# Kernel tuning notes

Hardware: AMD Instinct MI355X
Metric: run time of the kernel (lower is better)

The kernel has to match this reference:

```python
import jax, jax.numpy as jnp
import numpy as np

S = 3        # message passing steps
L = 128      # latent size
N = 10000    # nodes
E = 160000   # edges
DN, DE, DG = 64, 16, 8
OUT = 8
EPS = 1e-5


def _ln(x, scale, offset):
    m = jnp.mean(x, axis=-1, keepdims=True)
    v = jnp.var(x, axis=-1, keepdims=True)
    return (x - m) * jax.lax.rsqrt(v + EPS) * scale + offset


def _mlp(x, W0, b0, W1, b1):
    h = jax.nn.relu(x @ W0 + b0)
    return jax.nn.relu(h @ W1 + b1)


def setup_inputs() -> dict:
    key = jax.random.key(0)
    ks = iter(jax.random.split(key, 64))

    def w(shape, fan_in):
        return jax.random.normal(next(ks), shape, jnp.float32) / np.sqrt(fan_in).astype(np.float32)

    inp = {
        "nodes": jax.random.normal(next(ks), (N, DN), jnp.float32),
        "edges": jax.random.normal(next(ks), (E, DE), jnp.float32),
        "globals_": jax.random.normal(next(ks), (1, DG), jnp.float32),
        "senders": jax.random.randint(next(ks), (E,), 0, N),
        "receivers": jax.random.randint(next(ks), (E,), 0, N),
        # embedder
        "emb_node_W": w((DN, L), DN), "emb_node_b": jnp.zeros((L,), jnp.float32),
        "emb_edge_W": w((DE, L), DE), "emb_edge_b": jnp.zeros((L,), jnp.float32),
        "emb_glob_W": w((DG, L), DG), "emb_glob_b": jnp.zeros((L,), jnp.float32),
        # per-step MLPs (2 layers each)
        "edge_W0": w((S, 4 * L, L), 4 * L), "edge_b0": jnp.zeros((S, L), jnp.float32),
        "edge_W1": w((S, L, L), L),         "edge_b1": jnp.zeros((S, L), jnp.float32),
        "node_W0": w((S, 4 * L, L), 4 * L), "node_b0": jnp.zeros((S, L), jnp.float32),
        "node_W1": w((S, L, L), L),         "node_b1": jnp.zeros((S, L), jnp.float32),
        "glob_W0": w((S, 3 * L, L), 3 * L), "glob_b0": jnp.zeros((S, L), jnp.float32),
        "glob_W1": w((S, L, L), L),         "glob_b1": jnp.zeros((S, L), jnp.float32),
        # per-step layernorm (0: nodes, 1: edges, 2: globals)
        "ln_scale": jnp.ones((S, 3, L), jnp.float32),
        "ln_offset": jnp.zeros((S, 3, L), jnp.float32),
        # decoder (globals only)
        "dec_W": w((L, OUT), L), "dec_b": jnp.zeros((OUT,), jnp.float32),
    }
    return inp


def reference(nodes, edges, globals_, senders, receivers,
              emb_node_W, emb_node_b, emb_edge_W, emb_edge_b, emb_glob_W, emb_glob_b,
              edge_W0, edge_b0, edge_W1, edge_b1,
              node_W0, node_b0, node_W1, node_b1,
              glob_W0, glob_b0, glob_W1, glob_b1,
              ln_scale, ln_offset, dec_W, dec_b):
    # embed to latent
    n = nodes @ emb_node_W + emb_node_b      # [N, L]
    e = edges @ emb_edge_W + emb_edge_b      # [E, L]
    g = globals_ @ emb_glob_W + emb_glob_b   # [1, L]

    for s in range(S):
        # edge update: concat(edges, nodes[senders], nodes[receivers], globals)
        g_e = jnp.broadcast_to(g, (e.shape[0], L))
        e_in = jnp.concatenate([e, n[senders], n[receivers], g_e], axis=-1)  # [E, 4L]
        e_new = _mlp(e_in, edge_W0[s], edge_b0[s], edge_W1[s], edge_b1[s])
        # node update: concat(nodes, segsum(e,senders), segsum(e,receivers), globals)
        sent_agg = jax.ops.segment_sum(e_new, senders, num_segments=N)
        recv_agg = jax.ops.segment_sum(e_new, receivers, num_segments=N)
        g_n = jnp.broadcast_to(g, (N, L))
        n_in = jnp.concatenate([n, sent_agg, recv_agg, g_n], axis=-1)  # [N, 4L]
        n_new = _mlp(n_in, node_W0[s], node_b0[s], node_W1[s], node_b1[s])
        # global update: concat(node_agg, edge_agg, globals) (single graph)
        node_agg = jnp.sum(n_new, axis=0, keepdims=True)
        edge_agg = jnp.sum(e_new, axis=0, keepdims=True)
        g_in = jnp.concatenate([node_agg, edge_agg, g], axis=-1)  # [1, 3L]
        g_new = _mlp(g_in, glob_W0[s], glob_b0[s], glob_W1[s], glob_b1[s])
        # residual + layernorm
        n = _ln(n_new + n, ln_scale[s, 0], ln_offset[s, 0])
        e = _ln(e_new + e, ln_scale[s, 1], ln_offset[s, 1])
        g = _ln(g_new + g, ln_scale[s, 2], ln_offset[s, 2])

    # decoder maps globals only
    return g @ dec_W + dec_b  # [1, OUT]
```

## Files before the change

### kernel.cpp

```cpp
#include <hip/hip_runtime.h>
#include <hip/hip_bf16.h>

typedef __bf16 bf16;
typedef __bf16 bf16x8 __attribute__((ext_vector_type(8)));
typedef __bf16 bf16x4 __attribute__((ext_vector_type(4)));
typedef float  f32x4  __attribute__((ext_vector_type(4)));

#define NL 128
#define NN 10000
#define NE 160000
#define LN_EPS 1e-5f

__device__ __forceinline__ f32x4 f4zero() {
    f32x4 v; v[0] = 0.f; v[1] = 0.f; v[2] = 0.f; v[3] = 0.f; return v;
}

__device__ __forceinline__ int swz_off(int row, int b) {
    return row * 256 + (b ^ ((row & 7) << 4));
}

__device__ __forceinline__ bf16x8 frag_ld(const bf16* base, int row, int kbyte) {
    return *reinterpret_cast<const bf16x8*>(
        reinterpret_cast<const char*>(base) + swz_off(row, kbyte));
}

template <int NT>
__device__ __forceinline__ void stage_img(const bf16* __restrict__ img, bf16* dst, int tid) {
    #pragma unroll
    for (int i = 0; i < 2048 / NT; ++i) {
        int byte = (i * NT + tid) * 16;
        *reinterpret_cast<bf16x8*>(reinterpret_cast<char*>(dst) + byte) =
            *reinterpret_cast<const bf16x8*>(reinterpret_cast<const char*>(img) + byte);
    }
}

template <int NT>
__device__ __forceinline__ void stage_img_ld(const bf16* __restrict__ img, bf16x8* r, int tid) {
    #pragma unroll
    for (int i = 0; i < 2048 / NT; ++i)
        r[i] = *reinterpret_cast<const bf16x8*>(reinterpret_cast<const char*>(img) +
                                                (i * NT + tid) * 16);
}
template <int NT>
__device__ __forceinline__ void stage_img_st(bf16* dst, const bf16x8* r, int tid) {
    #pragma unroll
    for (int i = 0; i < 2048 / NT; ++i)
        *reinterpret_cast<bf16x8*>(reinterpret_cast<char*>(dst) + (i * NT + tid) * 16) = r[i];
}

__device__ __forceinline__ void stage_rows16(const float* __restrict__ src0, bf16* sX,
                                             int wrow0, int lane) {
    int c8 = (lane & 15) * 8;
    #pragma unroll
    for (int i = 0; i < 4; ++i) {
        int sub = i * 4 + (lane >> 4);
        const float* src = src0 + (size_t)sub * 128 + c8;
        f32x4 a = *reinterpret_cast<const f32x4*>(src);
        f32x4 b = *reinterpret_cast<const f32x4*>(src + 4);
        bf16x8 v;
        v[0] = (bf16)a[0]; v[1] = (bf16)a[1]; v[2] = (bf16)a[2]; v[3] = (bf16)a[3];
        v[4] = (bf16)b[0]; v[5] = (bf16)b[1]; v[6] = (bf16)b[2]; v[7] = (bf16)b[3];
        *reinterpret_cast<bf16x8*>(reinterpret_cast<char*>(sX) + swz_off(wrow0 + sub, c8 * 2)) = v;
    }
}

__device__ __forceinline__ void mfma_16x128(const bf16* sA, const bf16* sB, int arow, int kq,
                                            f32x4 acc[8]) {
    #pragma unroll
    for (int kk = 0; kk < 4; ++kk) {
        bf16x8 af = frag_ld(sA, arow, kk * 64 + kq);
        #pragma unroll
        for (int t = 0; t < 8; ++t) {
            bf16x8 bfr = frag_ld(sB, t * 16 + (arow & 15), kk * 64 + kq);
            acc[t] = __builtin_amdgcn_mfma_f32_16x16x32_bf16(af, bfr, acc[t], 0, 0, 0);
        }
    }
}

__device__ __forceinline__ void acc_to_lds_bf16(bf16* sX, const f32x4 acc[8], int w, int lane) {
    int c0 = lane & 15;
    #pragma unroll
    for (int r = 0; r < 4; ++r) {
        int rl = w * 16 + (lane >> 4) * 4 + r;
        #pragma unroll
        for (int t = 0; t < 8; ++t) {
            int col = t * 16 + c0;
            *reinterpret_cast<bf16*>(reinterpret_cast<char*>(sX) + swz_off(rl, col * 2)) =
                (bf16)acc[t][r];
        }
    }
}

__device__ __forceinline__ void lds_rows_to_global_bf16(const bf16* sX, bf16* __restrict__ dst0,
                                                        int w, int lane) {
    int c8 = (lane & 15) * 8;
    #pragma unroll
    for (int i = 0; i < 4; ++i) {
        int sub = i * 4 + (lane >> 4);
        bf16x8 v = *reinterpret_cast<const bf16x8*>(
            reinterpret_cast<const char*>(sX) + swz_off(w * 16 + sub, c8 * 2));
        *reinterpret_cast<bf16x8*>(dst0 + (size_t)sub * 128 + c8) = v;
    }
}

__global__ void k_prep(const float* __restrict__ eW0, const float* __restrict__ eW1,
                       const float* __restrict__ nW0, const float* __restrict__ nW1,
                       bf16* __restrict__ imgs, const float* __restrict__ globals_,
                       const float* __restrict__ embW, const float* __restrict__ embB,
                       float* __restrict__ g, const float* __restrict__ eb0,
                       const float* __restrict__ nb0, float* __restrict__ gve,
                       float* __restrict__ gvn, int* __restrict__ deg,
                       float* __restrict__ eagg, float* __restrict__ nagg,
                       int* __restrict__ done) {
    const int b = blockIdx.x;
    const int tid = threadIdx.x;
    if (b < 24) {
        const int s = b >> 3, kind = b & 7;
        const float* src;
        if (kind < 3)       src = eW0 + (size_t)s * 512 * 128 + (size_t)kind * 128 * 128;
        else if (kind == 3) src = eW1 + (size_t)s * 128 * 128;
        else if (kind < 7)  src = nW0 + (size_t)s * 512 * 128 + (size_t)(kind - 4) * 128 * 128;
        else                src = nW1 + (size_t)s * 128 * 128;
        bf16* img = imgs + (size_t)b * 16384;
        for (int i = 0; i < 16; ++i) {
            int q = tid + i * 256;
            int col = q & 127;
            int k0 = (q >> 7) << 2;
            bf16x4 v;
            v[0] = (bf16)src[(k0 + 0) * 128 + col];
            v[1] = (bf16)src[(k0 + 1) * 128 + col];
            v[2] = (bf16)src[(k0 + 2) * 128 + col];
            v[3] = (bf16)src[(k0 + 3) * 128 + col];
            *reinterpret_cast<bf16x4*>(reinterpret_cast<char*>(img) + swz_off(col, k0 * 2)) = v;
        }
    } else if (b == 24) {
        __shared__ float sG[128];
        if (tid < 3) done[tid] = 0;
        if (tid < 128) {
            float a = embB[tid];
            #pragma unroll
            for (int k = 0; k < 8; ++k) a += globals_[k] * embW[k * 128 + tid];
            g[tid] = a;
            sG[tid] = a;
        }
        __syncthreads();
        if (tid < 128) {
            const float* eW0g = eW0 + 384 * 128;
            const float* nW0g = nW0 + 384 * 128;
            float ae = eb0[tid], an = nb0[tid];
            for (int k = 0; k < 128; ++k) {
                float gv = sG[k];
                ae += gv * eW0g[k * 128 + tid];
                an += gv * nW0g[k * 128 + tid];
            }
            gve[tid] = ae;
            gvn[tid] = an;
        }
    } else {
        for (int i = tid; i < 2 * NN; i += 256) deg[i] = 0;
        for (int i = tid; i < 8 * 128; i += 256) eagg[i] = 0.f;
        for (int i = tid; i < 4 * 128; i += 256) nagg[i] = 0.f;
    }
}


__global__ void k_hist(const int* __restrict__ senders, const int* __restrict__ receivers,
                       int* __restrict__ deg_s, int* __restrict__ deg_r) {
    int i = blockIdx.x * 256 + threadIdx.x;
    if (i < NE) {
        atomicAdd(&deg_s[senders[i]], 1);
        atomicAdd(&deg_r[receivers[i]], 1);
    }
}

__device__ void scan_arr(const int* __restrict__ deg, int* __restrict__ rs, int* __restrict__ cur,
                         int* sW, int* sRun) {
    const int tid = threadIdx.x, lane = tid & 63, wid = tid >> 6;
    if (tid == 0) *sRun = 0;
    __syncthreads();
    for (int base = 0; base < NN; base += 1024) {
        int i = base + tid;
        int orig = (i < NN) ? deg[i] : 0;
        int v = orig;
        #pragma unroll
        for (int off = 1; off < 64; off <<= 1) {
            int u = __shfl_up(v, off, 64);
            if (lane >= off) v += u;
        }
        if (lane == 63) sW[wid] = v;
        __syncthreads();
        if (wid == 0 && lane < 16) {
            int u = sW[lane];
            #pragma unroll
            for (int off = 1; off < 16; off <<= 1) {
                int t = __shfl_up(u, off, 16);
                if (lane >= off) u += t;
            }
            sW[lane] = u;
        }
        __syncthreads();
        int waveoff = (wid == 0) ? 0 : sW[wid - 1];
        int incl = v + waveoff + *sRun;
        if (i < NN) {
            rs[i + 1] = incl;
            cur[i] = incl - orig;
        }
        __syncthreads();
        if (tid == 1023) *sRun = incl;
        __syncthreads();
    }
    if (tid == 0) rs[0] = 0;
}

__global__ void k_scan(const int* __restrict__ deg_s, int* __restrict__ rs_s,
                       int* __restrict__ cur_s, const int* __restrict__ deg_r,
                       int* __restrict__ rs_r, int* __restrict__ cur_r) {
    __shared__ int sW[16];
    __shared__ int sRun;
    scan_arr(deg_s, rs_s, cur_s, sW, &sRun);
    __syncthreads();
    scan_arr(deg_r, rs_r, cur_r, sW, &sRun);
}

__global__ void k_scatter_s(const int* __restrict__ senders, const int* __restrict__ receivers,
                            int* __restrict__ cur_s, int* __restrict__ perm,
                            int* __restrict__ snd_s, int* __restrict__ rcv_s) {
    int i = blockIdx.x * 256 + threadIdx.x;
    if (i < NE) {
        int s = senders[i];
        int p = atomicAdd(&cur_s[s], 1);
        perm[p] = i;
        snd_s[p] = s;
        rcv_s[p] = receivers[i];
    }
}

__global__ void k_scatter_r(const int* __restrict__ rcv_s, int* __restrict__ cur_r,
                            int* __restrict__ csr_r) {
    int j = blockIdx.x * 256 + threadIdx.x;
    if (j < NE) {
        int r = rcv_s[j];
        int p = atomicAdd(&cur_r[r], 1);
        csr_r[p] = j;
    }
}


__global__ __launch_bounds__(256, 2) void k_embed_nodes(
    const float* __restrict__ nodes, const float* __restrict__ W, const float* __restrict__ b,
    float* __restrict__ n_out, const bf16* __restrict__ imgPs, const bf16* __restrict__ imgPr,
    bf16* __restrict__ nsW, bf16* __restrict__ nrW) {
    __shared__ __align__(16) char smem[81920];
    float* sWemb = (float*)smem;
    float* sB = (float*)(smem + 32768);
    bf16* sWa = (bf16*)smem;
    bf16* sWb = (bf16*)(smem + 32768);
    bf16* sX = (bf16*)(smem + 65536);
    const int tid = threadIdx.x;
    const int lane = tid & 63;
    const int w = tid >> 6;
    const int rowbase = blockIdx.x * 64;
    const bool wvalid = (rowbase + w * 16) < NN;

    for (int i = tid; i < 64 * 128; i += 256) sWemb[i] = W[i];
    if (tid < 128) sB[tid] = b[tid];
    __syncthreads();
    const int col = tid & 127;
    const int rh = tid >> 7;
    for (int i = 0; i < 32; ++i) {
        int row = rowbase + i * 2 + rh;
        if (row < NN) {
            const f32x4* x4 = reinterpret_cast<const f32x4*>(nodes + (size_t)row * 64);
            float a = sB[col];
            #pragma unroll
            for (int k4 = 0; k4 < 16; ++k4) {
                f32x4 xv = x4[k4];
                a += xv[0] * sWemb[(k4 * 4 + 0) * 128 + col];
                a += xv[1] * sWemb[(k4 * 4 + 1) * 128 + col];
                a += xv[2] * sWemb[(k4 * 4 + 2) * 128 + col];
                a += xv[3] * sWemb[(k4 * 4 + 3) * 128 + col];
            }
            n_out[(size_t)row * 128 + col] = a;
            *reinterpret_cast<bf16*>(reinterpret_cast<char*>(sX) +
                                     swz_off(i * 2 + rh, col * 2)) = (bf16)a;
        }
    }
    __syncthreads();
    stage_img<256>(imgPs, sWa, tid);
    stage_img<256>(imgPr, sWb, tid);
    __syncthreads();
    if (!wvalid) return;

    const int arow = w * 16 + (lane & 15);
    const int kq = (lane >> 4) * 16;
    f32x4 acc[8], acc2[8];
    #pragma unroll
    for (int t = 0; t < 8; ++t) { acc[t] = f4zero(); acc2[t] = f4zero(); }
    mfma_16x128(sX, sWa, arow, kq, acc);
    mfma_16x128(sX, sWb, arow, kq, acc2);

    acc_to_lds_bf16(sX, acc, w, lane);
    lds_rows_to_global_bf16(sX, nsW + (size_t)(rowbase + w * 16) * 128, w, lane);
    acc_to_lds_bf16(sX, acc2, w, lane);
    lds_rows_to_global_bf16(sX, nrW + (size_t)(rowbase + w * 16) * 128, w, lane);
}

__global__ void k_embed_edges(const float* __restrict__ edges, const int* __restrict__ perm,
                              const float* __restrict__ W, const float* __restrict__ b,
                              bf16* __restrict__ e_out) {
    __shared__ float sW[16 * 128];
    __shared__ float sB[128];
    const int tid = threadIdx.x;
    for (int i = tid; i < 16 * 128; i += 256) sW[i] = W[i];
    if (tid < 128) sB[tid] = b[tid];
    __syncthreads();
    const int col = tid & 127;
    const int rh = tid >> 7;
    const int rowbase = blockIdx.x * 128;
    for (int i = 0; i < 64; ++i) {
        int row = rowbase + i * 2 + rh;
        int src = perm[row];
        const float* x = edges + (size_t)src * 16;
        float a = sB[col];
        #pragma unroll
        for (int k = 0; k < 16; ++k) a += x[k] * sW[k * 128 + col];
        e_out[(size_t)row * 128 + col] = (bf16)a;
    }
}


__global__ __launch_bounds__(512, 2) void k_edge(
    bf16* e_rw, bf16* __restrict__ e_new_out, const bf16* __restrict__ nsW,
    const bf16* __restrict__ nrW, float* __restrict__ edge_agg,
    const int* __restrict__ snd_s, const int* __restrict__ rcv_s,
    const bf16* __restrict__ imgW0, const bf16* __restrict__ imgW1,
    const float* __restrict__ gvec, const float* __restrict__ b1,
    const float* __restrict__ lnS, const float* __restrict__ lnO) {
    __shared__ __align__(16) char smem[65536];
    bf16* sW = (bf16*)smem;
    bf16* sX = (bf16*)(smem + 32768);
    float* sEagg = (float*)smem;

    const int tid = threadIdx.x;
    const int lane = tid & 63;
    const int w = tid >> 6;
    const int rowbase = blockIdx.x * 128;
    const int arow = w * 16 + (lane & 15);
    const int kq = (lane >> 4) * 16;
    const int c0 = lane & 15;
    const int qrt = lane >> 4;
    const int c8 = c0 * 8;

    stage_img<512>(imgW0, sW, tid);

    int snd_i[4], rcv_i[4];
    bf16x8 eold8[4];
    #pragma unroll
    for (int i = 0; i < 4; ++i) {
        int gr = rowbase + w * 16 + i * 4 + qrt;
        snd_i[i] = snd_s[gr];
        rcv_i[i] = rcv_s[gr];
        eold8[i] = *reinterpret_cast<const bf16x8*>(e_rw + (size_t)gr * 128 + c8);
    }

    f32x4 gvA = *reinterpret_cast<const f32x4*>(gvec + c8);
    f32x4 gvB = *reinterpret_cast<const f32x4*>(gvec + c8 + 4);
    f32x4 lsA = *reinterpret_cast<const f32x4*>(lnS + c8);
    f32x4 lsB = *reinterpret_cast<const f32x4*>(lnS + c8 + 4);
    f32x4 loA = *reinterpret_cast<const f32x4*>(lnO + c8);
    f32x4 loB = *reinterpret_cast<const f32x4*>(lnO + c8 + 4);
    float bb[8];
    #pragma unroll
    for (int t = 0; t < 8; ++t) bb[t] = b1[t * 16 + c0];

    bf16x8 ns8[4], nr8[4];
    #pragma unroll
    for (int i = 0; i < 4; ++i) {
        ns8[i] = *reinterpret_cast<const bf16x8*>(nsW + (size_t)snd_i[i] * 128 + c8);
        nr8[i] = *reinterpret_cast<const bf16x8*>(nrW + (size_t)rcv_i[i] * 128 + c8);
    }

    #pragma unroll
    for (int i = 0; i < 4; ++i)
        *reinterpret_cast<bf16x8*>(reinterpret_cast<char*>(sX) +
                                   swz_off(w * 16 + i * 4 + qrt, c8 * 2)) = eold8[i];

    __syncthreads();

    f32x4 acc[8];
    #pragma unroll
    for (int t = 0; t < 8; ++t) acc[t] = f4zero();
    __builtin_amdgcn_s_setprio(1);
    mfma_16x128(sX, sW, arow, kq, acc);
    __builtin_amdgcn_s_setprio(0);

    __syncthreads();

    bf16x8 w1r[4];
    stage_img_ld<512>(imgW1, w1r, tid);

    #pragma unroll
    for (int r = 0; r < 4; ++r) {
        int rl = w * 16 + (lane >> 4) * 4 + r;
        #pragma unroll
        for (int t = 0; t < 8; ++t)
            *reinterpret_cast<bf16*>(reinterpret_cast<char*>(sX) +
                                     swz_off(rl, (t * 16 + c0) * 2)) = (bf16)acc[t][r];
    }
    #pragma unroll
    for (int i = 0; i < 4; ++i) {
        int rl = w * 16 + i * 4 + qrt;
        bf16x8 a8 = *reinterpret_cast<const bf16x8*>(
            reinterpret_cast<const char*>(sX) + swz_off(rl, c8 * 2));
        bf16x8 h8;
        #pragma unroll
        for (int j = 0; j < 8; ++j) {
            float gvj = (j < 4) ? gvA[j] : gvB[j - 4];
            float v = (float)a8[j] + (float)ns8[i][j] + (float)nr8[i][j] + gvj;
            h8[j] = (bf16)fmaxf(v, 0.f);
        }
        *reinterpret_cast<bf16x8*>(reinterpret_cast<char*>(sX) + swz_off(rl, c8 * 2)) = h8;
    }

    stage_img_st<512>(sW, w1r, tid);
    __syncthreads();

    f32x4 acc2[8];
    #pragma unroll
    for (int t = 0; t < 8; ++t) acc2[t] = f4zero();
    __builtin_amdgcn_s_setprio(1);
    mfma_16x128(sX, sW, arow, kq, acc2);
    __builtin_amdgcn_s_setprio(0);

    #pragma unroll
    for (int r = 0; r < 4; ++r) {
        int rl = w * 16 + (lane >> 4) * 4 + r;
        #pragma unroll
        for (int t = 0; t < 8; ++t)
            *reinterpret_cast<bf16*>(reinterpret_cast<char*>(sX) +
                                     swz_off(rl, (t * 16 + c0) * 2)) =
                (bf16)fmaxf(acc2[t][r] + bb[t], 0.f);
    }

    float cs[8];
    #pragma unroll
    for (int j = 0; j < 8; ++j) cs[j] = 0.f;
    bf16* enew0 = e_new_out + (size_t)rowbase * 128;
    bf16* e0 = e_rw + (size_t)rowbase * 128;
    #pragma unroll
    for (int i = 0; i < 4; ++i) {
        int sub = w * 16 + i * 4 + qrt;
        bf16x8 en8 = *reinterpret_cast<const bf16x8*>(
            reinterpret_cast<const char*>(sX) + swz_off(sub, c8 * 2));
        *reinterpret_cast<bf16x8*>(enew0 + (size_t)sub * 128 + c8) = en8;
        float rv[8], s1 = 0.f, s2 = 0.f;
        #pragma unroll
        for (int j = 0; j < 8; ++j) {
            float en = (float)en8[j];
            cs[j] += en;
            float v = en + (float)eold8[i][j];
            rv[j] = v;
            s1 += v;
            s2 += v * v;
        }
        #pragma unroll
        for (int off = 1; off < 16; off <<= 1) {
            s1 += __shfl_xor(s1, off, 16);
            s2 += __shfl_xor(s2, off, 16);
        }
        float mean = s1 * (1.f / 128.f);
        float rstd = rsqrtf(s2 * (1.f / 128.f) - mean * mean + LN_EPS);
        bf16x8 o8;
        #pragma unroll
        for (int j = 0; j < 8; ++j) {
            float ls = (j < 4) ? lsA[j] : lsB[j - 4];
            float lo = (j < 4) ? loA[j] : loB[j - 4];
            o8[j] = (bf16)((rv[j] - mean) * rstd * ls + lo);
        }
        *reinterpret_cast<bf16x8*>(e0 + (size_t)sub * 128 + c8) = o8;
    }

    #pragma unroll
    for (int j = 0; j < 8; ++j) {
        cs[j] += __shfl_xor(cs[j], 16, 64);
        cs[j] += __shfl_xor(cs[j], 32, 64);
    }
    __syncthreads();
    if (qrt == 0) {
        float* dst = sEagg + w * 128 + c8;
        #pragma unroll
        for (int j = 0; j < 8; ++j) dst[j] = cs[j];
    }
    __syncthreads();
    if (tid < 128) {
        float v = 0.f;
        #pragma unroll
        for (int ww = 0; ww < 8; ++ww) v += sEagg[ww * 128 + tid];
        atomicAdd(&edge_agg[(blockIdx.x & 7) * 128 + tid], v);
    }
}

__global__ __launch_bounds__(256, 2) void k_node(
    float* n_rw, const bf16* __restrict__ e_new, const int* __restrict__ rs_s,
    const int* __restrict__ rs_r, const int* __restrict__ csr_r,
    float* __restrict__ node_agg , const bf16* __restrict__ imgW0,
    const bf16* __restrict__ imgW1, const float* __restrict__ gvec,
    const float* __restrict__ b1, const float* __restrict__ lnS,
    const float* __restrict__ lnO, const bf16* __restrict__ imgPs,
    const bf16* __restrict__ imgPr, bf16* __restrict__ nsW, bf16* __restrict__ nrW,
    int do_proj,
    int* __restrict__ done_ctr, float* __restrict__ edge_agg , float* __restrict__ g,
    const float* __restrict__ gW0, const float* __restrict__ gb0,
    const float* __restrict__ gW1, const float* __restrict__ gb1,
    const float* __restrict__ glnS, const float* __restrict__ glnO,
    const float* __restrict__ eW0g, const float* __restrict__ eb0n,
    const float* __restrict__ nW0g, const float* __restrict__ nb0n,
    float* __restrict__ gve, float* __restrict__ gvn, const float* __restrict__ decW,
    const float* __restrict__ decb, float* __restrict__ out, int do_next, int do_dec) {
    __shared__ __align__(16) char smem[81920];
    __shared__ int sLast;
    bf16* sA = (bf16*)smem;
    bf16* sB = (bf16*)(smem + 32768);
    bf16* sX = (bf16*)(smem + 65536);
    float* sNagg = (float*)smem;

    const int tid = threadIdx.x;
    const int lane = tid & 63;
    const int w = tid >> 6;
    const int rowbase = blockIdx.x * 64;
    const bool wvalid = (rowbase + w * 16) < NN;
    const int arow = w * 16 + (lane & 15);
    const int kq = (lane >> 4) * 16;
    const int c0 = lane & 15;
    const int qrt = lane >> 4;
    const int c8 = c0 * 8;

    stage_img<256>(imgW0, sA, tid);
    stage_img<256>(imgW0 + 16384, sB, tid);
    if (wvalid) stage_rows16(n_rw + (size_t)(rowbase + w * 16) * 128, sX, w * 16, lane);
    __syncthreads();

    float gvf[8], bbf[8];
    #pragma unroll
    for (int t = 0; t < 8; ++t) {
        gvf[t] = gvec[t * 16 + c0];
        bbf[t] = b1[t * 16 + c0];
    }
    f32x4 lsA4 = *reinterpret_cast<const f32x4*>(lnS + c8);
    f32x4 lsB4 = *reinterpret_cast<const f32x4*>(lnS + c8 + 4);
    f32x4 loA4 = *reinterpret_cast<const f32x4*>(lnO + c8);
    f32x4 loB4 = *reinterpret_cast<const f32x4*>(lnO + c8 + 4);

    f32x4 acc[8];
    #pragma unroll
    for (int t = 0; t < 8; ++t) acc[t] = f4zero();
    float cs[8];
    #pragma unroll
    for (int j = 0; j < 8; ++j) cs[j] = 0.f;

    if (wvalid) mfma_16x128(sX, sA, arow, kq, acc);
    __syncthreads();

    stage_img<256>(imgW0 + 32768, sA, tid);
    if (wvalid) {
        #pragma unroll
        for (int i = 0; i < 4; ++i) {
            int node = rowbase + w * 16 + i * 4 + qrt;
            float a[8];
            #pragma unroll
            for (int j = 0; j < 8; ++j) a[j] = 0.f;
            int jb = rs_s[node], je = rs_s[node + 1];
            int jj = jb;
            for (; jj + 3 < je; jj += 4) {
                bf16x8 v0 = *reinterpret_cast<const bf16x8*>(e_new + (size_t)(jj + 0) * 128 + c8);
                bf16x8 v1 = *reinterpret_cast<const bf16x8*>(e_new + (size_t)(jj + 1) * 128 + c8);
                bf16x8 v2 = *reinterpret_cast<const bf16x8*>(e_new + (size_t)(jj + 2) * 128 + c8);
                bf16x8 v3 = *reinterpret_cast<const bf16x8*>(e_new + (size_t)(jj + 3) * 128 + c8);
                #pragma unroll
                for (int j = 0; j < 8; ++j)
                    a[j] += (float)v0[j] + (float)v1[j] + (float)v2[j] + (float)v3[j];
            }
            for (; jj < je; ++jj) {
                bf16x8 v = *reinterpret_cast<const bf16x8*>(e_new + (size_t)jj * 128 + c8);
                #pragma unroll
                for (int j = 0; j < 8; ++j) a[j] += (float)v[j];
            }
            bf16x8 o;
            #pragma unroll
            for (int j = 0; j < 8; ++j) o[j] = (bf16)a[j];
            *reinterpret_cast<bf16x8*>(reinterpret_cast<char*>(sX) +
                                       swz_off(w * 16 + i * 4 + qrt, c8 * 2)) = o;
        }
        mfma_16x128(sX, sB, arow, kq, acc);
    }
    __syncthreads();

    stage_img<256>(imgW1, sB, tid);
    if (wvalid) {
        #pragma unroll
        for (int i = 0; i < 4; ++i) {
            int node = rowbase + w * 16 + i * 4 + qrt;
            float a[8];
            #pragma unroll
            for (int j = 0; j < 8; ++j) a[j] = 0.f;
            int pb = rs_r[node], pe = rs_r[node + 1];
            int pp = pb;
            for (; pp + 3 < pe; pp += 4) {
                int j0 = csr_r[pp], j1 = csr_r[pp + 1], j2 = csr_r[pp + 2], j3 = csr_r[pp + 3];
                bf16x8 v0 = *reinterpret_cast<const bf16x8*>(e_new + (size_t)j0 * 128 + c8);
                bf16x8 v1 = *reinterpret_cast<const bf16x8*>(e_new + (size_t)j1 * 128 + c8);
                bf16x8 v2 = *reinterpret_cast<const bf16x8*>(e_new + (size_t)j2 * 128 + c8);
                bf16x8 v3 = *reinterpret_cast<const bf16x8*>(e_new + (size_t)j3 * 128 + c8);
                #pragma unroll
                for (int j = 0; j < 8; ++j)
                    a[j] += (float)v0[j] + (float)v1[j] + (float)v2[j] + (float)v3[j];
            }
            for (; pp < pe; ++pp) {
                int j0 = csr_r[pp];
                bf16x8 v = *reinterpret_cast<const bf16x8*>(e_new + (size_t)j0 * 128 + c8);
                #pragma unroll
                for (int j = 0; j < 8; ++j) a[j] += (float)v[j];
            }
            bf16x8 o;
            #pragma unroll
            for (int j = 0; j < 8; ++j) o[j] = (bf16)a[j];
            *reinterpret_cast<bf16x8*>(reinterpret_cast<char*>(sX) +
                                       swz_off(w * 16 + i * 4 + qrt, c8 * 2)) = o;
        }
        mfma_16x128(sX, sA, arow, kq, acc);

        #pragma unroll
        for (int r = 0; r < 4; ++r) {
            int rl = w * 16 + (lane >> 4) * 4 + r;
            #pragma unroll
            for (int t = 0; t < 8; ++t)
                *reinterpret_cast<bf16*>(reinterpret_cast<char*>(sX) +
                                         swz_off(rl, (t * 16 + c0) * 2)) =
                    (bf16)fmaxf(acc[t][r] + gvf[t], 0.f);
        }
    }
    __syncthreads();

    if (wvalid) {
        #pragma unroll
        for (int t = 0; t < 8; ++t) acc[t] = f4zero();
        mfma_16x128(sX, sB, arow, kq, acc);
        #pragma unroll
        for (int r = 0; r < 4; ++r) {
            int rl = w * 16 + (lane >> 4) * 4 + r;
            #pragma unroll
            for (int t = 0; t < 8; ++t)
                *reinterpret_cast<bf16*>(reinterpret_cast<char*>(sX) +
                                         swz_off(rl, (t * 16 + c0) * 2)) =
                    (bf16)fmaxf(acc[t][r] + bbf[t], 0.f);
        }

        const float* nbase = n_rw + (size_t)(rowbase + w * 16) * 128;
        #pragma unroll
        for (int i = 0; i < 4; ++i) {
            int sub = i * 4 + qrt;
            bf16x8 en8 = *reinterpret_cast<const bf16x8*>(
                reinterpret_cast<const char*>(sX) + swz_off(w * 16 + sub, c8 * 2));
            f32x4 noA = *reinterpret_cast<const f32x4*>(nbase + (size_t)sub * 128 + c8);
            f32x4 noB = *reinterpret_cast<const f32x4*>(nbase + (size_t)sub * 128 + c8 + 4);
            float rv[8], s1 = 0.f, s2 = 0.f;
            #pragma unroll
            for (int j = 0; j < 8; ++j) {
                float en = (float)en8[j];
                cs[j] += en;
                float v = en + ((j < 4) ? noA[j] : noB[j - 4]);
                rv[j] = v;
                s1 += v;
                s2 += v * v;
            }
            #pragma unroll
            for (int off = 1; off < 16; off <<= 1) {
                s1 += __shfl_xor(s1, off, 16);
                s2 += __shfl_xor(s2, off, 16);
            }
            float mean = s1 * (1.f / 128.f);
            float rstd = rsqrtf(s2 * (1.f / 128.f) - mean * mean + LN_EPS);
            f32x4 oA, oB;
            bf16x8 l8;
            #pragma unroll
            for (int j = 0; j < 8; ++j) {
                float ls = (j < 4) ? lsA4[j] : lsB4[j - 4];
                float lo = (j < 4) ? loA4[j] : loB4[j - 4];
                float o = (rv[j] - mean) * rstd * ls + lo;
                if (j < 4) oA[j] = o; else oB[j - 4] = o;
                l8[j] = (bf16)o;
            }
            float* orow = n_rw + (size_t)(rowbase + w * 16 + sub) * 128 + c8;
            *reinterpret_cast<f32x4*>(orow) = oA;
            *reinterpret_cast<f32x4*>(orow + 4) = oB;
            *reinterpret_cast<bf16x8*>(reinterpret_cast<char*>(sX) +
                                       swz_off(w * 16 + sub, c8 * 2)) = l8;
        }
    }

    if (do_proj) {
        __syncthreads();
        stage_img<256>(imgPs, sA, tid);
        stage_img<256>(imgPr, sB, tid);
        __syncthreads();
        if (wvalid) {
            f32x4 pa[8], pb[8];
            #pragma unroll
            for (int t = 0; t < 8; ++t) { pa[t] = f4zero(); pb[t] = f4zero(); }
            mfma_16x128(sX, sA, arow, kq, pa);
            mfma_16x128(sX, sB, arow, kq, pb);
            acc_to_lds_bf16(sX, pa, w, lane);
            lds_rows_to_global_bf16(sX, nsW + (size_t)(rowbase + w * 16) * 128, w, lane);
            acc_to_lds_bf16(sX, pb, w, lane);
            lds_rows_to_global_bf16(sX, nrW + (size_t)(rowbase + w * 16) * 128, w, lane);
        }
    }

    #pragma unroll
    for (int j = 0; j < 8; ++j) {
        cs[j] += __shfl_xor(cs[j], 16, 64);
        cs[j] += __shfl_xor(cs[j], 32, 64);
    }
    __syncthreads();
    if (qrt == 0) {
        float* dst = sNagg + w * 128 + c8;
        #pragma unroll
        for (int j = 0; j < 8; ++j) dst[j] = wvalid ? cs[j] : 0.f;
    }
    __syncthreads();
    if (tid < 128) {
        float v = sNagg[tid] + sNagg[128 + tid] + sNagg[256 + tid] + sNagg[384 + tid];
        atomicAdd(&node_agg[(blockIdx.x & 3) * 128 + tid], v);
    }

    __syncthreads();
    if (tid == 0) {
        __threadfence();
        int old = atomicAdd(done_ctr, 1);
        sLast = (old == (int)gridDim.x - 1);
    }
    __syncthreads();
    if (!sLast) return;

    float* sIn = (float*)smem;
    float* sP0 = sIn + 384;
    float* sP1 = sP0 + 128;
    float* sH = sP1 + 128;
    float* sG = sH + 128;
    float* sMR = sG + 128;
    const int j = tid & 127;
    const int part = tid >> 7;

    if (tid < 128) {
        float v = 0.f;
        #pragma unroll
        for (int c = 0; c < 4; ++c) v += atomicAdd(&node_agg[c * 128 + tid], 0.f);
        #pragma unroll
        for (int c = 0; c < 4; ++c) atomicExch(&node_agg[c * 128 + tid], 0.f);
        sIn[tid] = v;
        sIn[256 + tid] = g[tid];
    } else {
        float v = 0.f;
        #pragma unroll
        for (int c = 0; c < 8; ++c) v += edge_agg[c * 128 + j];
        #pragma unroll
        for (int c = 0; c < 8; ++c) edge_agg[c * 128 + j] = 0.f;
        sIn[128 + j] = v;
    }
    __syncthreads();
    {
        float p = 0.f;
        for (int k = 0; k < 192; ++k) {
            int kk = part * 192 + k;
            p += sIn[kk] * gW0[(size_t)kk * 128 + j];
        }
        (part ? sP1 : sP0)[j] = p;
    }
    __syncthreads();
    if (tid < 128) sH[tid] = fmaxf(gb0[tid] + sP0[tid] + sP1[tid], 0.f);
    __syncthreads();
    {
        float p = 0.f;
        for (int k = 0; k < 64; ++k) {
            int kk = part * 64 + k;
            p += sH[kk] * gW1[(size_t)kk * 128 + j];
        }
        (part ? sP1 : sP0)[j] = p;
    }
    __syncthreads();
    float res = 0.f;
    if (tid < 128) {
        res = fmaxf(gb1[tid] + sP0[tid] + sP1[tid], 0.f) + sIn[256 + tid];
        sP0[tid] = res;
        sP1[tid] = res * res;
    }
    __syncthreads();
    if (tid < 64) {
        float a = sP0[tid] + sP0[tid + 64];
        float q = sP1[tid] + sP1[tid + 64];
        #pragma unroll
        for (int off = 1; off < 64; off <<= 1) {
            a += __shfl_xor(a, off, 64);
            q += __shfl_xor(q, off, 64);
        }
        if (tid == 0) {
            float m = a * (1.f / 128.f);
            float v = q * (1.f / 128.f) - m * m;
            sMR[0] = m;
            sMR[1] = rsqrtf(v + LN_EPS);
        }
    }
    __syncthreads();
    if (tid < 128) {
        float go = (res - sMR[0]) * sMR[1] * glnS[tid] + glnO[tid];
        g[tid] = go;
        sG[tid] = go;
    }
    __syncthreads();
    if (do_next) {
        float pe = 0.f, pn = 0.f;
        for (int k = 0; k < 64; ++k) {
            int kk = part * 64 + k;
            float gv = sG[kk];
            pe += gv * eW0g[(size_t)kk * 128 + j];
            pn += gv * nW0g[(size_t)kk * 128 + j];
        }
        (part ? sP1 : sP0)[j] = pe;
        sIn[part * 128 + j] = pn;
        __syncthreads();
        if (tid < 128) {
            gve[tid] = eb0n[tid] + sP0[tid] + sP1[tid];
            gvn[tid] = nb0n[tid] + sIn[tid] + sIn[128 + tid];
        }
    }
    if (do_dec && tid < 8) {
        float a = decb[tid];
        for (int k = 0; k < 128; ++k) a += sG[k] * decW[k * 8 + tid];
        out[tid] = a;
    }
}

extern "C" void kernel_launch(void* const* d_in, const int* in_sizes, int n_in, void* d_out,
                              int out_size, void* d_ws, size_t ws_size, hipStream_t stream) {
    (void)in_sizes; (void)n_in; (void)out_size; (void)ws_size;
    const float* nodes = (const float*)d_in[0];
    const float* edges = (const float*)d_in[1];
    const float* globals_ = (const float*)d_in[2];
    const int* senders = (const int*)d_in[3];
    const int* receivers = (const int*)d_in[4];
    const float* emb_node_W = (const float*)d_in[5];
    const float* emb_node_b = (const float*)d_in[6];
    const float* emb_edge_W = (const float*)d_in[7];
    const float* emb_edge_b = (const float*)d_in[8];
    const float* emb_glob_W = (const float*)d_in[9];
    const float* emb_glob_b = (const float*)d_in[10];
    const float* edge_W0 = (const float*)d_in[11];
    const float* edge_b0 = (const float*)d_in[12];
    const float* edge_W1 = (const float*)d_in[13];
    const float* edge_b1 = (const float*)d_in[14];
    const float* node_W0 = (const float*)d_in[15];
    const float* node_b0 = (const float*)d_in[16];
    const float* node_W1 = (const float*)d_in[17];
    const float* node_b1 = (const float*)d_in[18];
    const float* glob_W0 = (const float*)d_in[19];
    const float* glob_b0 = (const float*)d_in[20];
    const float* glob_W1 = (const float*)d_in[21];
    const float* glob_b1 = (const float*)d_in[22];
    const float* ln_scale = (const float*)d_in[23];
    const float* ln_offset = (const float*)d_in[24];
    const float* dec_W = (const float*)d_in[25];
    const float* dec_b = (const float*)d_in[26];

    char* ws = (char*)d_ws;
    size_t off = 0;
    auto alloc = [&](size_t bytes) -> char* {
        char* p = ws + off;
        off += (bytes + 255) & ~(size_t)255;
        return p;
    };
    bf16* e = (bf16*)alloc((size_t)NE * NL * 2);
    bf16* e_new = (bf16*)alloc((size_t)NE * NL * 2);
    float* n = (float*)alloc((size_t)NN * NL * 4);
    bf16* nsW = (bf16*)alloc((size_t)NN * NL * 2);
    bf16* nrW = (bf16*)alloc((size_t)NN * NL * 2);
    bf16* imgs = (bf16*)alloc((size_t)24 * 16384 * 2);
    float* eagg = (float*)alloc(8 * 128 * 4);
    float* nagg = (float*)alloc(4 * 128 * 4);
    float* g = (float*)alloc(128 * 4);
    float* gve = (float*)alloc(128 * 4);
    float* gvn = (float*)alloc(128 * 4);
    int* done = (int*)alloc(16 * 4);
    int* deg = (int*)alloc((size_t)2 * NN * 4);
    int* deg_s = deg;
    int* deg_r = deg + NN;
    int* rs_s = (int*)alloc((size_t)(NN + 1) * 4);
    int* rs_r = (int*)alloc((size_t)(NN + 1) * 4);
    int* cur_s = (int*)alloc((size_t)NN * 4);
    int* cur_r = (int*)alloc((size_t)NN * 4);
    int* perm = (int*)alloc((size_t)NE * 4);
    int* snd_s = (int*)alloc((size_t)NE * 4);
    int* rcv_s = (int*)alloc((size_t)NE * 4);
    int* csr_r = (int*)alloc((size_t)NE * 4);

    const int NB_N = (NN + 63) / 64;
    const int NB_E = NE / 128;
    const int NB_EMB = NE / 128;
    const int NB_SC = (NE + 255) / 256;

    auto img = [&](int s, int kind) -> const bf16* {
        return imgs + ((size_t)s * 8 + kind) * 16384;
    };

    k_prep<<<26, 256, 0, stream>>>(edge_W0, edge_W1, node_W0, node_W1, imgs, globals_,
                                   emb_glob_W, emb_glob_b, g, edge_b0, node_b0, gve, gvn,
                                   deg, eagg, nagg, done);

    k_hist<<<NB_SC, 256, 0, stream>>>(senders, receivers, deg_s, deg_r);
    k_scan<<<1, 1024, 0, stream>>>(deg_s, rs_s, cur_s, deg_r, rs_r, cur_r);
    k_scatter_s<<<NB_SC, 256, 0, stream>>>(senders, receivers, cur_s, perm, snd_s, rcv_s);
    k_scatter_r<<<NB_SC, 256, 0, stream>>>(rcv_s, cur_r, csr_r);

    k_embed_nodes<<<NB_N, 256, 0, stream>>>(nodes, emb_node_W, emb_node_b, n, img(0, 1),
                                            img(0, 2), nsW, nrW);
    k_embed_edges<<<NB_EMB, 256, 0, stream>>>(edges, perm, emb_edge_W, emb_edge_b, e);

    for (int s = 0; s < 3; ++s) {
        const int last = (s == 2);
        k_edge<<<NB_E, 512, 0, stream>>>(e, e_new, nsW, nrW, eagg, snd_s, rcv_s, img(s, 0),
                                         img(s, 3), gve, edge_b1 + s * 128,
                                         ln_scale + (s * 3 + 1) * 128,
                                         ln_offset + (s * 3 + 1) * 128);
        const float* eW0g = last ? edge_W0 : edge_W0 + (size_t)(s + 1) * 512 * 128 + 384 * 128;
        const float* eb0n = last ? edge_b0 : edge_b0 + (s + 1) * 128;
        const float* nW0g = last ? node_W0 : node_W0 + (size_t)(s + 1) * 512 * 128 + 384 * 128;
        const float* nb0n = last ? node_b0 : node_b0 + (s + 1) * 128;
        k_node<<<NB_N, 256, 0, stream>>>(
            n, e_new, rs_s, rs_r, csr_r, nagg, img(s, 4), img(s, 7), gvn, node_b1 + s * 128,
            ln_scale + (s * 3 + 0) * 128, ln_offset + (s * 3 + 0) * 128,
            img(last ? 0 : s + 1, 1), img(last ? 0 : s + 1, 2), nsW, nrW, !last,
            done + s, eagg, g, glob_W0 + (size_t)s * 384 * 128, glob_b0 + s * 128,
            glob_W1 + (size_t)s * 128 * 128, glob_b1 + s * 128, ln_scale + (s * 3 + 2) * 128,
            ln_offset + (s * 3 + 2) * 128, eW0g, eb0n, nW0g, nb0n, gve, gvn, dec_W, dec_b,
            (float*)d_out, !last, last);
    }
}
```

Baseline: 495.9 us.

## Split segment-sum aggregation out of node kernel into dedicated wide-parallel kernel

Moves the sender and receiver segment-sum gathers out of k_node into a new k_agg kernel with one wavefront per node, so each node's edges are split across four lane groups and combined with shuffle reductions. The sums are written to bf16 sent/recv buffers that k_node then loads directly into shared memory before its MFMA stages. The aim is to avoid the latency-bound serial gathers inside the occupancy-limited node kernel, which has 157 blocks of 256 threads, and to spread that work over 2500 blocks. The cost is an extra launch per step plus a write and re-read of two N x 128 bf16 buffers.

```diff
diff --git a/kernel.cpp b/kernel.cpp
--- a/kernel.cpp
+++ b/kernel.cpp
@@ -500,9 +500,61 @@
     }
 }
 
+__global__ __launch_bounds__(256) void k_agg(const bf16* __restrict__ e_new,
+                                             const int* __restrict__ rs_s,
+                                             const int* __restrict__ rs_r,
+                                             const int* __restrict__ csr_r,
+                                             bf16* __restrict__ sent, bf16* __restrict__ recv) {
+    const int lane = threadIdx.x & 63;
+    const int w = threadIdx.x >> 6;
+    const int node = blockIdx.x * 4 + w;
+    if (node >= NN) return;
+    const int qrt = lane >> 4;
+    const int c8 = (lane & 15) * 8;
+    float a[8];
+    #pragma unroll
+    for (int j = 0; j < 8; ++j) a[j] = 0.f;
+    const int b0 = rs_s[node], b1 = rs_s[node + 1];
+    for (int jj = b0 + qrt; jj < b1; jj += 4) {
+        bf16x8 v = *reinterpret_cast<const bf16x8*>(e_new + (size_t)jj * 128 + c8);
+        #pragma unroll
+        for (int j = 0; j < 8; ++j) a[j] += (float)v[j];
+    }
+    #pragma unroll
+    for (int j = 0; j < 8; ++j) {
+        a[j] += __shfl_xor(a[j], 16, 64);
+        a[j] += __shfl_xor(a[j], 32, 64);
+    }
+    if (qrt == 0) {
+        bf16x8 o;
+        #pragma unroll
+        for (int j = 0; j < 8; ++j) o[j] = (bf16)a[j];
+        *reinterpret_cast<bf16x8*>(sent + (size_t)node * 128 + c8) = o;
+    }
+    #pragma unroll
+    for (int j = 0; j < 8; ++j) a[j] = 0.f;
+    const int c1 = rs_r[node], c2 = rs_r[node + 1];
+    for (int pp = c1 + qrt; pp < c2; pp += 4) {
+        int jj = csr_r[pp];
+        bf16x8 v = *reinterpret_cast<const bf16x8*>(e_new + (size_t)jj * 128 + c8);
+        #pragma unroll
+        for (int j = 0; j < 8; ++j) a[j] += (float)v[j];
+    }
+    #pragma unroll
+    for (int j = 0; j < 8; ++j) {
+        a[j] += __shfl_xor(a[j], 16, 64);
+        a[j] += __shfl_xor(a[j], 32, 64);
+    }
+    if (qrt == 0) {
+        bf16x8 o;
+        #pragma unroll
+        for (int j = 0; j < 8; ++j) o[j] = (bf16)a[j];
+        *reinterpret_cast<bf16x8*>(recv + (size_t)node * 128 + c8) = o;
+    }
+}
+
 __global__ __launch_bounds__(256, 2) void k_node(
-    float* n_rw, const bf16* __restrict__ e_new, const int* __restrict__ rs_s,
-    const int* __restrict__ rs_r, const int* __restrict__ csr_r,
+    float* n_rw, const bf16* __restrict__ sent, const bf16* __restrict__ recv,
     float* __restrict__ node_agg , const bf16* __restrict__ imgW0,
     const bf16* __restrict__ imgW1, const float* __restrict__ gvec,
     const float* __restrict__ b1, const float* __restrict__ lnS,
@@ -537,7 +589,16 @@
 
     stage_img<256>(imgW0, sA, tid);
     stage_img<256>(imgW0 + 16384, sB, tid);
-    if (wvalid) stage_rows16(n_rw + (size_t)(rowbase + w * 16) * 128, sX, w * 16, lane);
+    bf16x8 sent8[4], recv8[4];
+    if (wvalid) {
+        stage_rows16(n_rw + (size_t)(rowbase + w * 16) * 128, sX, w * 16, lane);
+        #pragma unroll
+        for (int i = 0; i < 4; ++i) {
+            int gr = rowbase + w * 16 + i * 4 + qrt;
+            sent8[i] = *reinterpret_cast<const bf16x8*>(sent + (size_t)gr * 128 + c8);
+            recv8[i] = *reinterpret_cast<const bf16x8*>(recv + (size_t)gr * 128 + c8);
+        }
+    }
     __syncthreads();
 
     float gvf[8], bbf[8];
@@ -564,33 +625,9 @@
     stage_img<256>(imgW0 + 32768, sA, tid);
     if (wvalid) {
         #pragma unroll
-        for (int i = 0; i < 4; ++i) {
-            int node = rowbase + w * 16 + i * 4 + qrt;
-            float a[8];
-            #pragma unroll
-            for (int j = 0; j < 8; ++j) a[j] = 0.f;
-            int jb = rs_s[node], je = rs_s[node + 1];
-            int jj = jb;
-            for (; jj + 3 < je; jj += 4) {
-                bf16x8 v0 = *reinterpret_cast<const bf16x8*>(e_new + (size_t)(jj + 0) * 128 + c8);
-                bf16x8 v1 = *reinterpret_cast<const bf16x8*>(e_new + (size_t)(jj + 1) * 128 + c8);
-                bf16x8 v2 = *reinterpret_cast<const bf16x8*>(e_new + (size_t)(jj + 2) * 128 + c8);
-                bf16x8 v3 = *reinterpret_cast<const bf16x8*>(e_new + (size_t)(jj + 3) * 128 + c8);
-                #pragma unroll
-                for (int j = 0; j < 8; ++j)
-                    a[j] += (float)v0[j] + (float)v1[j] + (float)v2[j] + (float)v3[j];
-            }
-            for (; jj < je; ++jj) {
-                bf16x8 v = *reinterpret_cast<const bf16x8*>(e_new + (size_t)jj * 128 + c8);
-                #pragma unroll
-                for (int j = 0; j < 8; ++j) a[j] += (float)v[j];
-            }
-            bf16x8 o;
-            #pragma unroll
-            for (int j = 0; j < 8; ++j) o[j] = (bf16)a[j];
+        for (int i = 0; i < 4; ++i)
             *reinterpret_cast<bf16x8*>(reinterpret_cast<char*>(sX) +
-                                       swz_off(w * 16 + i * 4 + qrt, c8 * 2)) = o;
-        }
+                                       swz_off(w * 16 + i * 4 + qrt, c8 * 2)) = sent8[i];
         mfma_16x128(sX, sB, arow, kq, acc);
     }
     __syncthreads();
@@ -598,35 +635,9 @@
     stage_img<256>(imgW1, sB, tid);
     if (wvalid) {
         #pragma unroll
-        for (int i = 0; i < 4; ++i) {
-            int node = rowbase + w * 16 + i * 4 + qrt;
-            float a[8];
-            #pragma unroll
-            for (int j = 0; j < 8; ++j) a[j] = 0.f;
-            int pb = rs_r[node], pe = rs_r[node + 1];
-            int pp = pb;
-            for (; pp + 3 < pe; pp += 4) {
-                int j0 = csr_r[pp], j1 = csr_r[pp + 1], j2 = csr_r[pp + 2], j3 = csr_r[pp + 3];
-                bf16x8 v0 = *reinterpret_cast<const bf16x8*>(e_new + (size_t)j0 * 128 + c8);
-                bf16x8 v1 = *reinterpret_cast<const bf16x8*>(e_new + (size_t)j1 * 128 + c8);
-                bf16x8 v2 = *reinterpret_cast<const bf16x8*>(e_new + (size_t)j2 * 128 + c8);
-                bf16x8 v3 = *reinterpret_cast<const bf16x8*>(e_new + (size_t)j3 * 128 + c8);
-                #pragma unroll
-                for (int j = 0; j < 8; ++j)
-                    a[j] += (float)v0[j] + (float)v1[j] + (float)v2[j] + (float)v3[j];
-            }
-            for (; pp < pe; ++pp) {
-                int j0 = csr_r[pp];
-                bf16x8 v = *reinterpret_cast<const bf16x8*>(e_new + (size_t)j0 * 128 + c8);
-                #pragma unroll
-                for (int j = 0; j < 8; ++j) a[j] += (float)v[j];
-            }
-            bf16x8 o;
-            #pragma unroll
-            for (int j = 0; j < 8; ++j) o[j] = (bf16)a[j];
+        for (int i = 0; i < 4; ++i)
             *reinterpret_cast<bf16x8*>(reinterpret_cast<char*>(sX) +
-                                       swz_off(w * 16 + i * 4 + qrt, c8 * 2)) = o;
-        }
+                                       swz_off(w * 16 + i * 4 + qrt, c8 * 2)) = recv8[i];
         mfma_16x128(sX, sA, arow, kq, acc);
 
         #pragma unroll
@@ -883,6 +894,8 @@
     float* n = (float*)alloc((size_t)NN * NL * 4);
     bf16* nsW = (bf16*)alloc((size_t)NN * NL * 2);
     bf16* nrW = (bf16*)alloc((size_t)NN * NL * 2);
+    bf16* sent = (bf16*)alloc((size_t)NN * NL * 2);
+    bf16* recv = (bf16*)alloc((size_t)NN * NL * 2);
     bf16* imgs = (bf16*)alloc((size_t)24 * 16384 * 2);
     float* eagg = (float*)alloc(8 * 128 * 4);
     float* nagg = (float*)alloc(4 * 128 * 4);
@@ -906,6 +919,7 @@
     const int NB_E = NE / 128;
     const int NB_EMB = NE / 128;
     const int NB_SC = (NE + 255) / 256;
+    const int NB_AGG = NN / 4;
 
     auto img = [&](int s, int kind) -> const bf16* {
         return imgs + ((size_t)s * 8 + kind) * 16384;
@@ -930,12 +944,13 @@
                                          img(s, 3), gve, edge_b1 + s * 128,
                                          ln_scale + (s * 3 + 1) * 128,
                                          ln_offset + (s * 3 + 1) * 128);
+        k_agg<<<NB_AGG, 256, 0, stream>>>(e_new, rs_s, rs_r, csr_r, sent, recv);
         const float* eW0g = last ? edge_W0 : edge_W0 + (size_t)(s + 1) * 512 * 128 + 384 * 128;
         const float* eb0n = last ? edge_b0 : edge_b0 + (s + 1) * 128;
         const float* nW0g = last ? node_W0 : node_W0 + (size_t)(s + 1) * 512 * 128 + 384 * 128;
         const float* nb0n = last ? node_b0 : node_b0 + (s + 1) * 128;
         k_node<<<NB_N, 256, 0, stream>>>(
-            n, e_new, rs_s, rs_r, csr_r, nagg, img(s, 4), img(s, 7), gvn, node_b1 + s * 128,
+            n, sent, recv, nagg, img(s, 4), img(s, 7), gvn, node_b1 + s * 128,
             ln_scale + (s * 3 + 0) * 128, ln_offset + (s * 3 + 0) * 128,
             img(last ? 0 : s + 1, 1), img(last ? 0 : s + 1, 2), nsW, nrW, !last,
             done + s, eagg, g, glob_W0 + (size_t)s * 384 * 128, glob_b0 + s * 128,
```

Result: faster. 441.8 us (-10.9%).
